# Kernel tuning notes

Hardware: AMD Instinct MI355X
Metric: run time of the kernel (lower is better)

## Reference

```python
import jax, jax.numpy as jnp
import numpy as np

N_USERS = 100000
N_MOVIES = 100000
E = 1000000
D = 64
R = 5


def setup_inputs() -> dict:
    key = jax.random.key(0)
    k1, k2, k3, k4, k5 = jax.random.split(key, 5)
    z_user = jax.random.normal(k1, (N_USERS, D), dtype=jnp.float32)
    z_movie = jax.random.normal(k2, (N_MOVIES, D), dtype=jnp.float32)
    row = jax.random.randint(k3, (E,), 0, N_USERS)
    col = jax.random.randint(k4, (E,), 0, N_MOVIES)
    edge_label_index = jnp.stack([row, col], axis=0).astype(jnp.int64)
    Q = jax.random.normal(k5, (R, D, D), dtype=jnp.float32)
    return {"z_user": z_user, "z_movie": z_movie,
            "edge_label_index": edge_label_index, "Q": Q}


def reference(z_user, z_movie, edge_label_index, Q):
    row, col = edge_label_index[0], edge_label_index[1]
    u = z_user[row]        # [E, D] gathered user embeddings
    m = z_movie[col]       # [E, D] gathered movie embeddings
    # Per-edge bilinear form for each rating r: logit[e, r] = u_e^T Q_r m_e.
    # Equivalent to diag(U @ Q_r @ M^T) but O(E*D^2) instead of O(E^2*D).
    logits = jnp.einsum('ek,rkl,el->er', u, Q, m)  # [E, R]
    return jax.nn.log_softmax(logits, axis=-1)
```

## Files before the change

kernel.cpp:

```cpp
#include <hip/hip_runtime.h>
#include <stdint.h>

#define DD 64
#define RR 5

typedef float f32x4 __attribute__((ext_vector_type(4)));
typedef short short8 __attribute__((ext_vector_type(8)));

__device__ __forceinline__ unsigned short f2bf(float f) {
    union { float f; uint32_t u; } v; v.f = f;
    uint32_t u = v.u;
    u += 0x7FFFu + ((u >> 16) & 1u);
    return (unsigned short)(u >> 16);
}

__launch_bounds__(256, 2)
__global__ void bilinear_decoder_kernel(
    const float* __restrict__ z_user,
    const float* __restrict__ z_movie,
    const int*   __restrict__ eidx,
    const float* __restrict__ Qm,
    float*       __restrict__ out,
    int E)
{
    const int lane = threadIdx.x & 63;
    const int wid  = threadIdx.x >> 6;
    const int q    = lane >> 4;
    const int lm   = lane & 15;

    short8 Aq[RR][4][2];
#pragma unroll
    for (int r = 0; r < RR; ++r)
#pragma unroll
        for (int kt = 0; kt < 4; ++kt)
#pragma unroll
            for (int s = 0; s < 2; ++s) {
                const float* src = Qm + (((size_t)r * DD + kt * 16 + lm) * DD + s * 32 + q * 8);
                f32x4 a = *(const f32x4*)src;
                f32x4 b = *(const f32x4*)(src + 4);
                short8 h;
#pragma unroll
                for (int j = 0; j < 4; ++j) { h[j] = (short)f2bf(a[j]); h[4 + j] = (short)f2bf(b[j]); }
                Aq[r][kt][s] = h;
            }

    const int ngroups = (E + 15) >> 4;
    const int nw = gridDim.x << 2;
    for (int g = (blockIdx.x << 2) + wid; g < ngroups; g += nw) {
        const int base = g << 4;
        int e = base + lm;
        if (e >= E) e = E - 1;
        const int iu = eidx[e];
        const int im = eidx[E + e];
        const float* __restrict__ ur = z_user  + ((size_t)iu << 6);
        const float* __restrict__ mr = z_movie + ((size_t)im << 6);

        short8 Bm[2];
#pragma unroll
        for (int s = 0; s < 2; ++s) {
            f32x4 a = *(const f32x4*)(mr + s * 32 + q * 8);
            f32x4 b = *(const f32x4*)(mr + s * 32 + q * 8 + 4);
            short8 h;
#pragma unroll
            for (int j = 0; j < 4; ++j) { h[j] = (short)f2bf(a[j]); h[4 + j] = (short)f2bf(b[j]); }
            Bm[s] = h;
        }
        f32x4 uf[4];
#pragma unroll
        for (int kt = 0; kt < 4; ++kt)
            uf[kt] = *(const f32x4*)(ur + kt * 16 + q * 4);

        float lg[RR];
#pragma unroll
        for (int r = 0; r < RR; ++r) {
            f32x4 acc[4];
#pragma unroll
            for (int kt = 0; kt < 4; ++kt) {
                f32x4 c = {0.f, 0.f, 0.f, 0.f};
                c = __builtin_amdgcn_mfma_f32_16x16x32_bf16(Aq[r][kt][0], Bm[0], c, 0, 0, 0);
                c = __builtin_amdgcn_mfma_f32_16x16x32_bf16(Aq[r][kt][1], Bm[1], c, 0, 0, 0);
                acc[kt] = c;
            }
            float p = 0.f;
#pragma unroll
            for (int kt = 0; kt < 4; ++kt)
#pragma unroll
                for (int rg = 0; rg < 4; ++rg)
                    p = fmaf(uf[kt][rg], acc[kt][rg], p);
            p += __shfl_xor(p, 16);
            p += __shfl_xor(p, 32);
            lg[r] = p;
        }

        float mx = lg[0];
#pragma unroll
        for (int r = 1; r < RR; ++r) mx = fmaxf(mx, lg[r]);
        float sum = 0.f;
#pragma unroll
        for (int r = 0; r < RR; ++r) sum += __expf(lg[r] - mx);
        const float sub = mx + __logf(sum);

        if (base + lm < E) {
            const size_t o = (size_t)(base + lm) * RR;
            out[o + q] = lg[q] - sub;
            if (q == 0) out[o + 4] = lg[4] - sub;
        }
    }
}

extern "C" void kernel_launch(void* const* d_in, const int* in_sizes, int n_in,
                              void* d_out, int out_size, void* d_ws, size_t ws_size,
                              hipStream_t stream) {
    const float* z_user  = (const float*)d_in[0];
    const float* z_movie = (const float*)d_in[1];
    const int*   eidx    = (const int*)d_in[2];
    const float* Qm      = (const float*)d_in[3];
    float* out = (float*)d_out;

    const int E = in_sizes[2] / 2;
    const int ngroups = (E + 15) >> 4;
    int nblocks = (ngroups + 3) / 4;
    if (nblocks > 512) nblocks = 512;

    bilinear_decoder_kernel<<<nblocks, 256, 0, stream>>>(
        z_user, z_movie, eidx, Qm, out, E);
}
```

Baseline: 208.1 us.

## Software-pipeline gathers with double-buffered rows and coalesced LDS-staged output stores

Restructures the per-wave loop into a two-stage software pipeline: edge indices and embedding rows for the next groups are loaded into registers while the current group is computed, hiding gather latency. Output logits are staged through shared memory so each wave writes its 80 contiguous floats in coalesced stores. The bf16 conversion also switches to the native __bf16 cast, and an empty asm pins the Q fragments in registers. The cost is higher register pressure from two in-flight row buffers, and the LDS staging is used within a wave without an explicit barrier.

Measured after the change: 179.2 us. -13.9%, faster.

```diff
diff --git a/kernel.cpp b/kernel.cpp
--- a/kernel.cpp
+++ b/kernel.cpp
@@ -6,13 +6,21 @@
 
 typedef float f32x4 __attribute__((ext_vector_type(4)));
 typedef short short8 __attribute__((ext_vector_type(8)));
+typedef __bf16 bf16x8 __attribute__((ext_vector_type(8)));
 
-__device__ __forceinline__ unsigned short f2bf(float f) {
-    union { float f; uint32_t u; } v; v.f = f;
-    uint32_t u = v.u;
-    u += 0x7FFFu + ((u >> 16) & 1u);
-    return (unsigned short)(u >> 16);
+union BF8 { bf16x8 h; short8 s; };
+
+__device__ __forceinline__ short8 pack_bf16(f32x4 a, f32x4 b) {
+    BF8 u;
+#pragma unroll
+    for (int j = 0; j < 4; ++j) { u.h[j] = (__bf16)a[j]; u.h[4 + j] = (__bf16)b[j]; }
+    return u.s;
 }
+
+struct Rows {
+    f32x4 m0, m1, m2, m3;
+    f32x4 u0, u1, u2, u3;
+};
 
 __launch_bounds__(256, 2)
 __global__ void bilinear_decoder_kernel(
@@ -28,6 +36,8 @@
     const int q    = lane >> 4;
     const int lm   = lane & 15;
 
+    __shared__ float st_lds[4][80];
+
     short8 Aq[RR][4][2];
 #pragma unroll
     for (int r = 0; r < RR; ++r)
@@ -36,62 +46,62 @@
 #pragma unroll
             for (int s = 0; s < 2; ++s) {
                 const float* src = Qm + (((size_t)r * DD + kt * 16 + lm) * DD + s * 32 + q * 8);
-                f32x4 a = *(const f32x4*)src;
-                f32x4 b = *(const f32x4*)(src + 4);
-                short8 h;
+                Aq[r][kt][s] = pack_bf16(*(const f32x4*)src, *(const f32x4*)(src + 4));
+            }
 #pragma unroll
-                for (int j = 0; j < 4; ++j) { h[j] = (short)f2bf(a[j]); h[4 + j] = (short)f2bf(b[j]); }
-                Aq[r][kt][s] = h;
-            }
+    for (int r = 0; r < RR; ++r)
+#pragma unroll
+        for (int kt = 0; kt < 4; ++kt)
+#pragma unroll
+            for (int s = 0; s < 2; ++s)
+                asm volatile("" : "+v"(Aq[r][kt][s]));
 
     const int ngroups = (E + 15) >> 4;
     const int nw = gridDim.x << 2;
-    for (int g = (blockIdx.x << 2) + wid; g < ngroups; g += nw) {
-        const int base = g << 4;
-        int e = base + lm;
+    const int g0 = (blockIdx.x << 2) + wid;
+    if (g0 >= ngroups) return;
+    const int nsteps = (ngroups - 1 - g0) / nw + 1;
+
+    auto ld_idx = [&](int g, int& iu, int& im) {
+        int gg = g < ngroups ? g : (ngroups - 1);
+        int e = (gg << 4) + lm;
         if (e >= E) e = E - 1;
-        const int iu = eidx[e];
-        const int im = eidx[E + e];
-        const float* __restrict__ ur = z_user  + ((size_t)iu << 6);
-        const float* __restrict__ mr = z_movie + ((size_t)im << 6);
-
-        short8 Bm[2];
-#pragma unroll
-        for (int s = 0; s < 2; ++s) {
-            f32x4 a = *(const f32x4*)(mr + s * 32 + q * 8);
-            f32x4 b = *(const f32x4*)(mr + s * 32 + q * 8 + 4);
-            short8 h;
-#pragma unroll
-            for (int j = 0; j < 4; ++j) { h[j] = (short)f2bf(a[j]); h[4 + j] = (short)f2bf(b[j]); }
-            Bm[s] = h;
-        }
-        f32x4 uf[4];
-#pragma unroll
-        for (int kt = 0; kt < 4; ++kt)
-            uf[kt] = *(const f32x4*)(ur + kt * 16 + q * 4);
-
+        iu = eidx[e];
+        im = eidx[E + e];
+    };
+    auto ld_rows = [&](int iu, int im, Rows& R_) {
+        const float* mr = z_movie + ((size_t)im << 6);
+        const float* ur = z_user  + ((size_t)iu << 6);
+        R_.m0 = *(const f32x4*)(mr + q * 8);
+        R_.m1 = *(const f32x4*)(mr + q * 8 + 4);
+        R_.m2 = *(const f32x4*)(mr + 32 + q * 8);
+        R_.m3 = *(const f32x4*)(mr + 32 + q * 8 + 4);
+        R_.u0 = *(const f32x4*)(ur + q * 4);
+        R_.u1 = *(const f32x4*)(ur + 16 + q * 4);
+        R_.u2 = *(const f32x4*)(ur + 32 + q * 4);
+        R_.u3 = *(const f32x4*)(ur + 48 + q * 4);
+    };
+    auto compute = [&](const Rows& R_, int g, bool store) {
+        const short8 Bm0 = pack_bf16(R_.m0, R_.m1);
+        const short8 Bm1 = pack_bf16(R_.m2, R_.m3);
         float lg[RR];
 #pragma unroll
         for (int r = 0; r < RR; ++r) {
-            f32x4 acc[4];
+            float p = 0.f;
 #pragma unroll
             for (int kt = 0; kt < 4; ++kt) {
                 f32x4 c = {0.f, 0.f, 0.f, 0.f};
-                c = __builtin_amdgcn_mfma_f32_16x16x32_bf16(Aq[r][kt][0], Bm[0], c, 0, 0, 0);
-                c = __builtin_amdgcn_mfma_f32_16x16x32_bf16(Aq[r][kt][1], Bm[1], c, 0, 0, 0);
-                acc[kt] = c;
-            }
-            float p = 0.f;
-#pragma unroll
-            for (int kt = 0; kt < 4; ++kt)
+                c = __builtin_amdgcn_mfma_f32_16x16x32_bf16(Aq[r][kt][0], Bm0, c, 0, 0, 0);
+                c = __builtin_amdgcn_mfma_f32_16x16x32_bf16(Aq[r][kt][1], Bm1, c, 0, 0, 0);
+                const f32x4 uf = (kt == 0) ? R_.u0 : (kt == 1) ? R_.u1 : (kt == 2) ? R_.u2 : R_.u3;
 #pragma unroll
                 for (int rg = 0; rg < 4; ++rg)
-                    p = fmaf(uf[kt][rg], acc[kt][rg], p);
+                    p = fmaf(uf[rg], c[rg], p);
+            }
             p += __shfl_xor(p, 16);
             p += __shfl_xor(p, 32);
             lg[r] = p;
         }
-
         float mx = lg[0];
 #pragma unroll
         for (int r = 1; r < RR; ++r) mx = fmaxf(mx, lg[r]);
@@ -100,11 +110,37 @@
         for (int r = 0; r < RR; ++r) sum += __expf(lg[r] - mx);
         const float sub = mx + __logf(sum);
 
-        if (base + lm < E) {
-            const size_t o = (size_t)(base + lm) * RR;
-            out[o + q] = lg[q] - sub;
-            if (q == 0) out[o + 4] = lg[4] - sub;
+        const float v0 = (q == 0) ? lg[0] : (q == 1) ? lg[1] : (q == 2) ? lg[2] : lg[3];
+        st_lds[wid][lm * 5 + q] = v0 - sub;
+        if (q == 0) st_lds[wid][lm * 5 + 4] = lg[4] - sub;
+
+        if (store) {
+            const size_t o = (size_t)g * (16 * RR);
+            const size_t lim = (size_t)E * RR;
+            if (o + lane < lim)              out[o + lane]      = st_lds[wid][lane];
+            if (lane < 16 && o + 64 + lane < lim) out[o + 64 + lane] = st_lds[wid][64 + lane];
         }
+    };
+
+    int iuA, imA, iuB, imB;
+    Rows RA, RB;
+    int gA = g0;
+    int gB = g0 + nw;
+    ld_idx(gA, iuA, imA);
+    ld_rows(iuA, imA, RA);
+    ld_idx(gB, iuB, imB);
+
+    for (int i = 0; i < nsteps; i += 2) {
+        ld_rows(iuB, imB, RB);
+        ld_idx(gA + 2 * nw, iuA, imA);
+        compute(RA, gA, true);
+
+        ld_rows(iuA, imA, RA);
+        ld_idx(gB + 2 * nw, iuB, imB);
+        compute(RB, gB, (i + 1) < nsteps);
+
+        gA += 2 * nw;
+        gB += 2 * nw;
     }
 }
 
```

## Switch to 32x32 MFMA with LDS-resident Q, prefetch gathers, coalesced stores

Applied to the files above, without the earlier changes.

Processes 32 edges per wave using 32x32x16 bf16 MFMA instead of 16x16x32. The bf16 Q fragments are held in shared memory instead of registers, which frees registers so occupancy can rise to 3 blocks per SM. Movie/user row loads and edge indices are software-prefetched for the next group while the current group computes. Outputs are staged through LDS so each group writes 160 contiguous floats. The risks are added LDS read traffic for Q on every MFMA and a tail group that is not bounds-checked on store.

Result: slower. 360.0 us (+73.1%).

```diff
diff --git a/kernel.cpp b/kernel.cpp
--- a/kernel.cpp
+++ b/kernel.cpp
@@ -3,18 +3,23 @@
 
 #define DD 64
 #define RR 5
+#define NWAVES 4
+#define BLOCK 256
 
-typedef float f32x4 __attribute__((ext_vector_type(4)));
+typedef float f32x4  __attribute__((ext_vector_type(4)));
+typedef float f32x16 __attribute__((ext_vector_type(16)));
 typedef short short8 __attribute__((ext_vector_type(8)));
+typedef __bf16 bf16x8 __attribute__((ext_vector_type(8)));
+union BF8 { bf16x8 h; short8 s; };
 
-__device__ __forceinline__ unsigned short f2bf(float f) {
-    union { float f; uint32_t u; } v; v.f = f;
-    uint32_t u = v.u;
-    u += 0x7FFFu + ((u >> 16) & 1u);
-    return (unsigned short)(u >> 16);
+__device__ __forceinline__ short8 pack_bf16(f32x4 a, f32x4 b) {
+    BF8 u;
+#pragma unroll
+    for (int j = 0; j < 4; ++j) { u.h[j] = (__bf16)a[j]; u.h[4 + j] = (__bf16)b[j]; }
+    return u.s;
 }
 
-__launch_bounds__(256, 2)
+__launch_bounds__(BLOCK, 3)
 __global__ void bilinear_decoder_kernel(
     const float* __restrict__ z_user,
     const float* __restrict__ z_movie,
@@ -23,88 +28,115 @@
     float*       __restrict__ out,
     int E)
 {
-    const int lane = threadIdx.x & 63;
-    const int wid  = threadIdx.x >> 6;
-    const int q    = lane >> 4;
-    const int lm   = lane & 15;
+    __shared__ short8 qfrag[RR * 8][64];
+    __shared__ float  st[NWAVES][160];
 
-    short8 Aq[RR][4][2];
+    const int tid  = threadIdx.x;
+    const int wid  = tid >> 6;
+    const int lane = tid & 63;
+    const int e32  = lane & 31;
+    const int hi   = lane >> 5;
+
 #pragma unroll
-    for (int r = 0; r < RR; ++r)
+    for (int t = 0; t < 10; ++t) {
+        const int f  = wid * 10 + t;
+        const int r  = f >> 3;
+        const int kt = (f >> 2) & 1;
+        const int ks = f & 3;
+        const float* src = Qm + (((size_t)r * DD + kt * 32 + e32) * DD + ks * 16 + hi * 8);
+        qfrag[f][lane] = pack_bf16(*(const f32x4*)src, *(const f32x4*)(src + 4));
+    }
+    __syncthreads();
+
+    const int ng = (E + 31) >> 5;
+    const int NW = (int)gridDim.x * NWAVES;
+    int g = (int)blockIdx.x * NWAVES + wid;
+    if (g >= ng) return;
+
+    f32x4 mS[8];
+    f32x4 uS[8];
+    int iu_n, im_n;
+
+    auto ldidx = [&](int gg, int& a, int& b) {
+        gg = gg < ng ? gg : ng - 1;
+        int e = (gg << 5) + e32;
+        if (e >= E) e = E - 1;
+        a = eidx[e];
+        b = eidx[E + e];
+    };
+    auto issue_m = [&](int im) {
+        const float* mr = z_movie + ((size_t)im << 6);
 #pragma unroll
-        for (int kt = 0; kt < 4; ++kt)
+        for (int ks = 0; ks < 4; ++ks) {
+            mS[2 * ks]     = *(const f32x4*)(mr + ks * 16 + hi * 8);
+            mS[2 * ks + 1] = *(const f32x4*)(mr + ks * 16 + hi * 8 + 4);
+        }
+    };
+    auto issue_u = [&](int iu) {
+        const float* ur = z_user + ((size_t)iu << 6);
 #pragma unroll
-            for (int s = 0; s < 2; ++s) {
-                const float* src = Qm + (((size_t)r * DD + kt * 16 + lm) * DD + s * 32 + q * 8);
-                f32x4 a = *(const f32x4*)src;
-                f32x4 b = *(const f32x4*)(src + 4);
-                short8 h;
+        for (int kt = 0; kt < 2; ++kt)
 #pragma unroll
-                for (int j = 0; j < 4; ++j) { h[j] = (short)f2bf(a[j]); h[4 + j] = (short)f2bf(b[j]); }
-                Aq[r][kt][s] = h;
-            }
+            for (int g8 = 0; g8 < 4; ++g8)
+                uS[kt * 4 + g8] = *(const f32x4*)(ur + kt * 32 + g8 * 8 + hi * 4);
+    };
 
-    const int ngroups = (E + 15) >> 4;
-    const int nw = gridDim.x << 2;
-    for (int g = (blockIdx.x << 2) + wid; g < ngroups; g += nw) {
-        const int base = g << 4;
-        int e = base + lm;
-        if (e >= E) e = E - 1;
-        const int iu = eidx[e];
-        const int im = eidx[E + e];
-        const float* __restrict__ ur = z_user  + ((size_t)iu << 6);
-        const float* __restrict__ mr = z_movie + ((size_t)im << 6);
+    int iu0, im0;
+    ldidx(g, iu0, im0);
+    issue_m(im0);
+    issue_u(iu0);
+    ldidx(g + NW, iu_n, im_n);
 
-        short8 Bm[2];
-#pragma unroll
-        for (int s = 0; s < 2; ++s) {
-            f32x4 a = *(const f32x4*)(mr + s * 32 + q * 8);
-            f32x4 b = *(const f32x4*)(mr + s * 32 + q * 8 + 4);
-            short8 h;
-#pragma unroll
-            for (int j = 0; j < 4; ++j) { h[j] = (short)f2bf(a[j]); h[4 + j] = (short)f2bf(b[j]); }
-            Bm[s] = h;
-        }
-        f32x4 uf[4];
-#pragma unroll
-        for (int kt = 0; kt < 4; ++kt)
-            uf[kt] = *(const f32x4*)(ur + kt * 16 + q * 4);
+    for (; g < ng; g += NW) {
+        const short8 Bm0 = pack_bf16(mS[0], mS[1]);
+        const short8 Bm1 = pack_bf16(mS[2], mS[3]);
+        const short8 Bm2 = pack_bf16(mS[4], mS[5]);
+        const short8 Bm3 = pack_bf16(mS[6], mS[7]);
+        const int  iu_c = iu_n;
+        const bool more = (g + NW) < ng;
+        if (more) issue_m(im_n);
 
         float lg[RR];
 #pragma unroll
         for (int r = 0; r < RR; ++r) {
-            f32x4 acc[4];
-#pragma unroll
-            for (int kt = 0; kt < 4; ++kt) {
-                f32x4 c = {0.f, 0.f, 0.f, 0.f};
-                c = __builtin_amdgcn_mfma_f32_16x16x32_bf16(Aq[r][kt][0], Bm[0], c, 0, 0, 0);
-                c = __builtin_amdgcn_mfma_f32_16x16x32_bf16(Aq[r][kt][1], Bm[1], c, 0, 0, 0);
-                acc[kt] = c;
-            }
             float p = 0.f;
 #pragma unroll
-            for (int kt = 0; kt < 4; ++kt)
+            for (int kt = 0; kt < 2; ++kt) {
+                const int fb = (r * 2 + kt) * 4;
+                f32x16 acc = 0.f;
+                acc = __builtin_amdgcn_mfma_f32_32x32x16_bf16(qfrag[fb + 0][lane], Bm0, acc, 0, 0, 0);
+                acc = __builtin_amdgcn_mfma_f32_32x32x16_bf16(qfrag[fb + 1][lane], Bm1, acc, 0, 0, 0);
+                acc = __builtin_amdgcn_mfma_f32_32x32x16_bf16(qfrag[fb + 2][lane], Bm2, acc, 0, 0, 0);
+                acc = __builtin_amdgcn_mfma_f32_32x32x16_bf16(qfrag[fb + 3][lane], Bm3, acc, 0, 0, 0);
 #pragma unroll
-                for (int rg = 0; rg < 4; ++rg)
-                    p = fmaf(uf[kt][rg], acc[kt][rg], p);
-            p += __shfl_xor(p, 16);
+                for (int g8 = 0; g8 < 4; ++g8)
+#pragma unroll
+                    for (int j = 0; j < 4; ++j)
+                        p = fmaf(uS[kt * 4 + g8][j], acc[g8 * 4 + j], p);
+            }
             p += __shfl_xor(p, 32);
             lg[r] = p;
         }
+        if (more) { issue_u(iu_c); ldidx(g + 2 * NW, iu_n, im_n); }
 
-        float mx = lg[0];
+        float mx = fmaxf(fmaxf(fmaxf(lg[0], lg[1]), fmaxf(lg[2], lg[3])), lg[4]);
+        float s = 0.f;
 #pragma unroll
-        for (int r = 1; r < RR; ++r) mx = fmaxf(mx, lg[r]);
-        float sum = 0.f;
-#pragma unroll
-        for (int r = 0; r < RR; ++r) sum += __expf(lg[r] - mx);
-        const float sub = mx + __logf(sum);
+        for (int r = 0; r < RR; ++r) s += __expf(lg[r] - mx);
+        const float sub = mx + __logf(s);
 
-        if (base + lm < E) {
-            const size_t o = (size_t)(base + lm) * RR;
-            out[o + q] = lg[q] - sub;
-            if (q == 0) out[o + 4] = lg[4] - sub;
+        if (hi == 0) {
+            st[wid][e32 * 5 + 0] = lg[0] - sub;
+            st[wid][e32 * 5 + 1] = lg[1] - sub;
+            st[wid][e32 * 5 + 2] = lg[2] - sub;
+        } else {
+            st[wid][e32 * 5 + 3] = lg[3] - sub;
+            st[wid][e32 * 5 + 4] = lg[4] - sub;
         }
+        float* og = out + (size_t)g * 160;
+        og[lane]      = st[wid][lane];
+        og[64 + lane] = st[wid][64 + lane];
+        if (lane < 32) og[128 + lane] = st[wid][128 + lane];
     }
 }
 
@@ -118,10 +150,10 @@
     float* out = (float*)d_out;
 
     const int E = in_sizes[2] / 2;
-    const int ngroups = (E + 15) >> 4;
-    int nblocks = (ngroups + 3) / 4;
-    if (nblocks > 512) nblocks = 512;
+    const int ng = (E + 31) >> 5;
+    int nblocks = (ng + NWAVES - 1) / NWAVES;
+    if (nblocks > 768) nblocks = 768;
 
-    bilinear_decoder_kernel<<<nblocks, 256, 0, stream>>>(
+    bilinear_decoder_kernel<<<nblocks, BLOCK, 0, stream>>>(
         z_user, z_movie, eidx, Qm, out, E);
 }
```
